# Kernel tuning notes

Hardware: AMD Instinct MI355X
Metric: run time of the kernel (lower is better)

The kernel has to match this reference:

```python
import jax, jax.numpy as jnp
import numpy as np
import math

NHEAD = 8
OUT = 64
EF = 64
IN = 256
NTYPES = 5
NH = 50000
NT = 100000
E = 800000
NEG_SLOPE = 0.2

def _uniform(key, shape, fan):
    # matches reset(): uniform(-stdv, stdv), stdv = sqrt(6/(fan_in+fan_out)) over last two dims
    stdv = math.sqrt(6.0 / (shape[-2] + shape[-1]))
    return jax.random.uniform(key, shape, jnp.float32, -stdv, stdv)

def setup_inputs() -> dict:
    key = jax.random.key(0)
    ks = jax.random.split(key, 12)
    head_feature = jax.random.normal(ks[0], (NH, IN), jnp.float32)
    tail_feature = jax.random.normal(ks[1], (NT, IN), jnp.float32)
    head_ind = jax.random.randint(ks[2], (E,), 0, NH)
    tail_ind = jax.random.randint(ks[3], (E,), 0, NT)
    tmp_edge = jax.random.randint(ks[4], (E,), 0, NTYPES)
    edge_emb = _uniform(ks[5], (NTYPES, EF), None)
    W = _uniform(ks[6], (IN, OUT * NHEAD), None)
    W_e = _uniform(ks[7], (EF, EF * NHEAD), None)
    a_l = _uniform(ks[8], (1, NHEAD, OUT), None)
    a_r = _uniform(ks[9], (1, NHEAD, OUT), None)
    a_e = _uniform(ks[10], (1, NHEAD, EF), None)
    return {"head_feature": head_feature, "tail_feature": tail_feature,
            "head_ind": head_ind, "tail_ind": tail_ind, "tmp_edge": tmp_edge,
            "edge_emb": edge_emb, "W": W, "W_e": W_e,
            "a_l": a_l, "a_r": a_r, "a_e": a_e}

def reference(head_feature, tail_feature, head_ind, tail_ind, tmp_edge,
              edge_emb, W, W_e, a_l, a_r, a_e):
    n_head_nodes = head_feature.shape[0]
    # projections (dropout is identity in eval)
    h_head = (head_feature @ W).reshape(-1, NHEAD, OUT)   # [NH, H, D]
    h_tail = (tail_feature @ W).reshape(-1, NHEAD, OUT)   # [NT, H, D]
    e = (edge_emb @ W_e).reshape(-1, NHEAD, EF)           # [T, H, EF]
    # per-edge attention logits, all heads at once: [E, H]
    h_l = jnp.sum(a_l * h_head, axis=-1)[head_ind]
    h_r = jnp.sum(a_r * h_tail, axis=-1)[tail_ind]
    h_e = jnp.sum(a_e * e, axis=-1)[tmp_edge]
    att = jax.nn.leaky_relu(h_l + h_r + h_e, NEG_SLOPE)
    # sparse (per-destination-row) softmax, vectorized over heads
    seg_max = jax.ops.segment_max(att, head_ind, num_segments=n_head_nodes)
    att = jnp.exp(att - seg_max[head_ind])
    denom = jax.ops.segment_sum(att, head_ind, num_segments=n_head_nodes)
    att = att / denom[head_ind]                           # [E, H]
    # weighted aggregation per head (small fixed loop over heads)
    outs = [jax.ops.segment_sum(att[:, n:n + 1] * h_tail[tail_ind, n, :],
                                head_ind, num_segments=n_head_nodes)
            for n in range(NHEAD)]
    out = jnp.stack(outs, axis=1).reshape(n_head_nodes, -1)  # [NH, H*D]
    return out, att
```

## Files before the change

### kernel.cpp

```cpp
#include <hip/hip_runtime.h>

#define NH 50000
#define NT 100000
#define NE 800000
#define MPAD 100096

typedef __attribute__((ext_vector_type(8))) short bf16x8;
typedef __attribute__((ext_vector_type(4))) float f32x4;

__device__ __forceinline__ unsigned short f2bf(float f){
  unsigned int u = __float_as_uint(f);
  u += 0x7FFFu + ((u >> 16) & 1u);
  return (unsigned short)(u >> 16);
}

__device__ __forceinline__ void fma8(float* acc, float w, uint4 pk){
  acc[0] += w*__uint_as_float(pk.x<<16); acc[1] += w*__uint_as_float(pk.x&0xFFFF0000u);
  acc[2] += w*__uint_as_float(pk.y<<16); acc[3] += w*__uint_as_float(pk.y&0xFFFF0000u);
  acc[4] += w*__uint_as_float(pk.z<<16); acc[5] += w*__uint_as_float(pk.z&0xFFFF0000u);
  acc[6] += w*__uint_as_float(pk.w<<16); acc[7] += w*__uint_as_float(pk.w&0xFFFF0000u);
}

__global__ void k_prep(const float* __restrict__ W, const float* __restrict__ W_e,
                       const float* __restrict__ edge_emb,
                       const float* __restrict__ a_l, const float* __restrict__ a_r,
                       const float* __restrict__ a_e,
                       unsigned short* __restrict__ wlr_t,
                       float* __restrict__ h_e){
  __shared__ float s_al[512], s_ar[512], s_ae[512], s_wef[512];
  int t = threadIdx.x;
  for (int i=t;i<512;i+=256){ s_al[i]=a_l[i]; s_ar[i]=a_r[i]; s_ae[i]=a_e[i]; }
  __syncthreads();
  { int k = t;
    for (int h=0;h<8;h++){
      float accl=0.f, accr=0.f;
      for (int d=0; d<64; d++){
        float w = W[k*512 + h*64 + d];
        accl += w*s_al[h*64+d];
        accr += w*s_ar[h*64+d];
      }
      wlr_t[h*256 + k]     = f2bf(accl);
      wlr_t[(8+h)*256 + k] = f2bf(accr);
    }
  }
  if (t<64){
    for (int h=0;h<8;h++){
      float acc=0.f;
      for (int f=0; f<64; f++) acc += W_e[t*512 + h*64 + f]*s_ae[h*64+f];
      s_wef[t*8+h]=acc;
    }
  }
  __syncthreads();
  if (t<40){
    int ty=t>>3, h=t&7;
    float acc=0.f;
    for (int k2=0;k2<64;k2++) acc += edge_emb[ty*64+k2]*s_wef[k2*8+h];
    h_e[t]=acc;
  }
}

__global__ void k_wt(const float* __restrict__ W, unsigned short* __restrict__ Wt){
  int n = blockIdx.x, k = threadIdx.x;
  Wt[n*256+k] = f2bf(W[k*512+n]);
}

__global__ __launch_bounds__(256) void k_hlr2(const float* __restrict__ head_f,
      const float* __restrict__ tail_f, const unsigned short* __restrict__ wlr_t,
      float* __restrict__ h_l, float* __restrict__ h_r){
  __shared__ unsigned short As[256*64];
  __shared__ unsigned short Bs[16*256];
  int t = threadIdx.x;
  int wave = t>>6, lane = t&63;
  int lr = lane&15, lq = lane>>4;
  long r0 = (long)blockIdx.x*256;

#pragma unroll
  for (int i=0;i<2;i++){
    int q = i*256 + t;
    int c = q>>5, un = q&31;
    float4 v = *(const float4*)(wlr_t + c*256 + un*8);
    int u = un ^ (c&7);
    *(float4*)((char*)Bs + c*512 + u*16) = v;
  }

  f32x4 acc[4];
#pragma unroll
  for (int mf=0;mf<4;mf++) acc[mf]=(f32x4){0.f,0.f,0.f,0.f};

  for (int kt=0; kt<4; kt++){
    __syncthreads();
#pragma unroll
    for (int i=0;i<16;i++){
      int q = i*256+t;
      int row = q>>4, cg = q&15;
      long gr = r0 + row;
      float4 v = make_float4(0.f,0.f,0.f,0.f);
      if (gr < NH) v = *(const float4*)(head_f + gr*256 + kt*64 + cg*4);
      else if (gr < NH+NT) v = *(const float4*)(tail_f + (gr-NH)*256 + kt*64 + cg*4);
      int u = (cg>>1) ^ (row&7);
      ushort4 sv;
      sv.x=f2bf(v.x); sv.y=f2bf(v.y); sv.z=f2bf(v.z); sv.w=f2bf(v.w);
      *(ushort4*)((char*)As + row*128 + u*16 + (cg&1)*8) = sv;
    }
    __syncthreads();
#pragma unroll
    for (int ks=0;ks<2;ks++){
      int un = kt*8 + ks*4 + lq;
      int cu = un ^ (lr&7);
      bf16x8 bfr = *(const bf16x8*)((const char*)Bs + lr*512 + cu*16);
#pragma unroll
      for (int mf=0;mf<4;mf++){
        int r = wave*64 + mf*16 + lr;
        int u = (ks*4+lq) ^ (r&7);
        bf16x8 afr = *(const bf16x8*)((const char*)As + r*128 + u*16);
        acc[mf] = __builtin_amdgcn_mfma_f32_16x16x32_bf16(afr, bfr, acc[mf], 0,0,0);
      }
    }
  }
#pragma unroll
  for (int mf=0;mf<4;mf++)
#pragma unroll
    for (int j=0;j<4;j++){
      long grow = r0 + wave*64 + mf*16 + lq*4 + j;
      float v = acc[mf][j];
      if (grow < NH){ if (lr<8) h_l[grow*8+lr] = v; }
      else if (grow < NH+NT){ if (lr>=8) h_r[(grow-NH)*8+lr-8] = v; }
    }
}

__global__ __launch_bounds__(256) void k_gemm(const float* __restrict__ Aref,
      const unsigned short* __restrict__ Wt, unsigned short* __restrict__ Cout){
  __shared__ unsigned short As[128*64];
  __shared__ unsigned short Bs[128*64];
  int t = threadIdx.x;
  int m0 = blockIdx.x*128;
  int n0 = blockIdx.y*128;
  int wave = t>>6, lane = t&63;
  int wm = (wave>>1)*64, wn = (wave&1)*64;
  int lr = lane & 15, lq = lane >> 4;

  f32x4 acc[4][4];
#pragma unroll
  for (int mf=0;mf<4;mf++)
#pragma unroll
    for (int nf=0;nf<4;nf++) acc[mf][nf] = (f32x4){0.f,0.f,0.f,0.f};

  for (int kt=0; kt<4; kt++){
#pragma unroll
    for (int i=0;i<8;i++){
      int q = i*256 + t;
      int row = q>>4;
      int cg  = q&15;
      int grow = m0 + row;
      float4 v = make_float4(0.f,0.f,0.f,0.f);
      if (grow < NT) v = *(const float4*)(Aref + (size_t)grow*256 + kt*64 + cg*4);
      int u  = (cg>>1) ^ (row&7);
      ushort4 sv;
      sv.x=f2bf(v.x); sv.y=f2bf(v.y); sv.z=f2bf(v.z); sv.w=f2bf(v.w);
      *(ushort4*)((char*)As + row*128 + u*16 + (cg&1)*8) = sv;
    }
#pragma unroll
    for (int i=0;i<4;i++){
      int q = i*256 + t;
      int row = q>>3;
      int un  = q&7;
      float4 v = *(const float4*)(Wt + (size_t)(n0+row)*256 + kt*64 + un*8);
      int u = un ^ (row&7);
      *(float4*)((char*)Bs + row*128 + u*16) = v;
    }
    __syncthreads();

    bf16x8 af[2][4], bfr[2][4];
#pragma unroll
    for (int ks=0;ks<2;ks++)
#pragma unroll
      for (int mf=0;mf<4;mf++){
        int r = wm + mf*16 + lr;
        int u = (ks*4 + lq) ^ (r&7);
        af[ks][mf] = *(const bf16x8*)((const char*)As + r*128 + u*16);
      }
#pragma unroll
    for (int ks=0;ks<2;ks++)
#pragma unroll
      for (int nf=0;nf<4;nf++){
        int c = wn + nf*16 + lr;
        int u = (ks*4 + lq) ^ (c&7);
        bfr[ks][nf] = *(const bf16x8*)((const char*)Bs + c*128 + u*16);
      }
#pragma unroll
    for (int ks=0;ks<2;ks++)
#pragma unroll
      for (int mf=0;mf<4;mf++)
#pragma unroll
        for (int nf=0;nf<4;nf++)
          acc[mf][nf] = __builtin_amdgcn_mfma_f32_16x16x32_bf16(af[ks][mf], bfr[ks][nf], acc[mf][nf], 0,0,0);
    __syncthreads();
  }
#pragma unroll
  for (int mf=0;mf<4;mf++)
#pragma unroll
    for (int nf=0;nf<4;nf++){
      int gr = m0 + wm + mf*16 + lq*4;
      int gc = n0 + wn + nf*16 + lr;
#pragma unroll
      for (int j=0;j<4;j++)
        Cout[(size_t)(gr+j)*512 + gc] = f2bf(acc[mf][nf][j]);
    }
}

__global__ void k_hist(const int* __restrict__ head_ind, int* __restrict__ cnt){
  int e = blockIdx.x*256 + threadIdx.x;
  atomicAdd(&cnt[head_ind[e]], 1);
}

__global__ void k_scan1(const int* __restrict__ cnt, int* __restrict__ bsum){
  __shared__ int s[256];
  int b=blockIdx.x, t=threadIdx.x, g=b*256+t;
  s[t] = (g<NH)? cnt[g] : 0;
  __syncthreads();
  for (int off=128; off>0; off>>=1){ if (t<off) s[t]+=s[t+off]; __syncthreads(); }
  if (t==0) bsum[b]=s[0];
}
__global__ void k_scan2(int* __restrict__ bsum, int nb){
  __shared__ int s[256];
  int t=threadIdx.x;
  int v = (t<nb)? bsum[t] : 0;
  s[t]=v; __syncthreads();
  for (int off=1; off<256; off<<=1){
    int u = (t>=off)? s[t-off] : 0; __syncthreads();
    s[t]+=u; __syncthreads();
  }
  if (t<nb) bsum[t] = s[t]-v;
}
__global__ void k_scan3(const int* __restrict__ cnt, const int* __restrict__ bsum,
                        int* __restrict__ offs, int* __restrict__ cur){
  __shared__ int s[256];
  int b=blockIdx.x, t=threadIdx.x, g=b*256+t;
  int v=(g<NH)? cnt[g] : 0;
  s[t]=v; __syncthreads();
  for (int off=1; off<256; off<<=1){
    int u=(t>=off)? s[t-off] : 0; __syncthreads();
    s[t]+=u; __syncthreads();
  }
  int excl = s[t]-v + bsum[b];
  if (g<NH){
    offs[g]=excl; cur[g]=excl;
    if (g==NH-1) offs[NH]=excl+v;
  }
}

__global__ void k_logit2(const int* __restrict__ head_ind, const int* __restrict__ tail_ind,
                         const int* __restrict__ tmp_edge,
                         const float* __restrict__ h_l, const float* __restrict__ h_r,
                         const float* __restrict__ h_e,
                         int* __restrict__ cur,
                         float* __restrict__ att, float* __restrict__ att_csr,
                         int* __restrict__ edge_of, int* __restrict__ tail_s){
  int g = blockIdx.x*256 + threadIdx.x;
  int e = g>>3, h = g&7, l = threadIdx.x&63;
  int hd = head_ind[e], tl = tail_ind[e], ty = tmp_edge[e];
  float v = h_l[hd*8+h] + h_r[tl*8+h] + h_e[ty*8+h];
  v = v > 0.f ? v : 0.2f*v;
  att[g] = v;
  int p = 0;
  if (h==0) p = atomicAdd(&cur[hd], 1);
  p = __shfl(p, l & ~7);
  att_csr[p*8+h] = v;
  if (h==0){ edge_of[p]=e; tail_s[p]=tl; }
}

__global__ __launch_bounds__(256) void k_agg3(const int* __restrict__ offs,
      const int* __restrict__ edge_of, const int* __restrict__ tail_s,
      const float* __restrict__ att_csr,
      const unsigned short* __restrict__ h_tail,
      float* __restrict__ att, float* __restrict__ out){
  int t = threadIdx.x;
  int l = t & 63;
  int i = blockIdx.x*4 + (t>>6);
  int h = l & 7, hq = l >> 3;
  int s0 = offs[i];
  int deg = offs[i+1] - s0;

  float m = -1e30f;
  for (int q = hq; q < deg; q += 8) m = fmaxf(m, att_csr[(s0+q)*8 + h]);
  m = fmaxf(m, __shfl_xor(m, 8));
  m = fmaxf(m, __shfl_xor(m, 16));
  m = fmaxf(m, __shfl_xor(m, 32));
  float sum = 0.f;
  for (int q = hq; q < deg; q += 8) sum += __expf(att_csr[(s0+q)*8 + h] - m);
  sum += __shfl_xor(sum, 8); sum += __shfl_xor(sum, 16); sum += __shfl_xor(sum, 32);
  float r = (deg > 0) ? 1.f/sum : 0.f;

  for (int q = hq; q < deg; q += 8){
    int p = s0 + q;
    float a = __expf(att_csr[p*8 + h] - m) * r;
    int e = edge_of[p];
    att[(size_t)e*8 + h] = a;
  }

  float mh = __shfl(m, hq), rh = __shfl(r, hq);
  float acc[8];
#pragma unroll
  for (int c=0;c<8;c++) acc[c]=0.f;
  int j = 0;
  for (; j+2 <= deg; j += 2){
    int p0 = s0+j, p1 = s0+j+1;
    int t0 = tail_s[p0], t1 = tail_s[p1];
    float a0 = att_csr[p0*8 + hq], a1 = att_csr[p1*8 + hq];
    uint4 r0 = *(const uint4*)(h_tail + (size_t)t0*512 + l*8);
    uint4 r1 = *(const uint4*)(h_tail + (size_t)t1*512 + l*8);
    float w0 = __expf(a0 - mh) * rh;
    float w1 = __expf(a1 - mh) * rh;
    fma8(acc, w0, r0);
    fma8(acc, w1, r1);
  }
  if (j < deg){
    int p0 = s0+j;
    int t0 = tail_s[p0];
    float a0 = att_csr[p0*8 + hq];
    uint4 r0 = *(const uint4*)(h_tail + (size_t)t0*512 + l*8);
    float w0 = __expf(a0 - mh) * rh;
    fma8(acc, w0, r0);
  }
  float* o = out + (size_t)i*512 + l*8;
  *(float4*)o     = make_float4(acc[0],acc[1],acc[2],acc[3]);
  *(float4*)(o+4) = make_float4(acc[4],acc[5],acc[6],acc[7]);
}

extern "C" void kernel_launch(void* const* d_in, const int* in_sizes, int n_in,
                              void* d_out, int out_size, void* d_ws, size_t ws_size,
                              hipStream_t stream) {
  const float* head_f   = (const float*)d_in[0];
  const float* tail_f   = (const float*)d_in[1];
  const int*   head_ind = (const int*)d_in[2];
  const int*   tail_ind = (const int*)d_in[3];
  const int*   tmp_edge = (const int*)d_in[4];
  const float* edge_emb = (const float*)d_in[5];
  const float* W        = (const float*)d_in[6];
  const float* W_e      = (const float*)d_in[7];
  const float* a_l      = (const float*)d_in[8];
  const float* a_r      = (const float*)d_in[9];
  const float* a_e      = (const float*)d_in[10];

  float* out = (float*)d_out;
  float* att = out + (size_t)NH*512;

  char* ws = (char*)d_ws;
  auto alloc = [&](size_t bytes)->char*{ char* p = ws; ws += (bytes+511)&~(size_t)511; return p; };
  unsigned short* Wt    = (unsigned short*)alloc((size_t)512*256*2);
  unsigned short* wlr_t = (unsigned short*)alloc((size_t)16*256*2);
  float* h_e            = (float*)alloc(512);
  float* h_l            = (float*)alloc((size_t)NH*8*4);
  float* h_r            = (float*)alloc((size_t)NT*8*4);
  unsigned short* h_tail= (unsigned short*)alloc((size_t)MPAD*512*2);
  int* cnt              = (int*)alloc((size_t)NH*4);
  int* offs             = (int*)alloc((size_t)(NH+1)*4);
  int* cur              = (int*)alloc((size_t)NH*4);
  int* bsum             = (int*)alloc(1024);
  int* edge_of          = (int*)alloc((size_t)NE*4);
  int* tail_s           = (int*)alloc((size_t)NE*4);
  float* att_csr        = (float*)alloc((size_t)NE*8*4);

  hipMemsetAsync(cnt, 0, (size_t)NH*4, stream);
  k_prep<<<1,256,0,stream>>>(W, W_e, edge_emb, a_l, a_r, a_e, wlr_t, h_e);
  k_wt<<<512,256,0,stream>>>(W, Wt);
  k_hlr2<<<(NH+NT+255)/256,256,0,stream>>>(head_f, tail_f, wlr_t, h_l, h_r);
  k_gemm<<<dim3(MPAD/128,4),256,0,stream>>>(tail_f, Wt, h_tail);
  k_hist<<<NE/256,256,0,stream>>>(head_ind, cnt);
  k_scan1<<<196,256,0,stream>>>(cnt, bsum);
  k_scan2<<<1,256,0,stream>>>(bsum, 196);
  k_scan3<<<196,256,0,stream>>>(cnt, bsum, offs, cur);
  k_logit2<<<NE*8/256,256,0,stream>>>(head_ind, tail_ind, tmp_edge, h_l, h_r, h_e,
                                      cur, att, att_csr, edge_of, tail_s);
  k_agg3<<<NH/4,256,0,stream>>>(offs, edge_of, tail_s, att_csr, h_tail, att, out);
}
```

Measured before the change: 465.9 us.

## Fuse tail attention logits into projection GEMM epilogue and merge att writes into aggregation

The tail-side logit h_r is now computed in the k_gemm epilogue as a dot product of the fp32 accumulators with a_r, reduced with lane shuffles. This removes the 100k tail rows from k_hlr2, so the tail features are not read a second time. The redundant att write in k_logit2 and the separate normalization pass in k_agg3 are removed; normalized weights are written with nontemporal stores inside the aggregation loop, which is unrolled to 4 edges. h_r now comes from fp32 accumulators instead of a bf16 folded weight, which slightly changes numerics. There is also a bug risk: k_gemm runs over MPAD rows and guards with gr<NT, which is fine, but one write lane per head group issues scattered stores.

```diff
diff --git a/kernel.cpp b/kernel.cpp
--- a/kernel.cpp
+++ b/kernel.cpp
@@ -64,9 +64,8 @@
   Wt[n*256+k] = f2bf(W[k*512+n]);
 }
 
-__global__ __launch_bounds__(256) void k_hlr2(const float* __restrict__ head_f,
-      const float* __restrict__ tail_f, const unsigned short* __restrict__ wlr_t,
-      float* __restrict__ h_l, float* __restrict__ h_r){
+__global__ __launch_bounds__(256) void k_hl(const float* __restrict__ head_f,
+      const unsigned short* __restrict__ wlr_t, float* __restrict__ h_l){
   __shared__ unsigned short As[256*64];
   __shared__ unsigned short Bs[16*256];
   int t = threadIdx.x;
@@ -96,7 +95,6 @@
       long gr = r0 + row;
       float4 v = make_float4(0.f,0.f,0.f,0.f);
       if (gr < NH) v = *(const float4*)(head_f + gr*256 + kt*64 + cg*4);
-      else if (gr < NH+NT) v = *(const float4*)(tail_f + (gr-NH)*256 + kt*64 + cg*4);
       int u = (cg>>1) ^ (row&7);
       ushort4 sv;
       sv.x=f2bf(v.x); sv.y=f2bf(v.y); sv.z=f2bf(v.z); sv.w=f2bf(v.w);
@@ -122,14 +120,13 @@
 #pragma unroll
     for (int j=0;j<4;j++){
       long grow = r0 + wave*64 + mf*16 + lq*4 + j;
-      float v = acc[mf][j];
-      if (grow < NH){ if (lr<8) h_l[grow*8+lr] = v; }
-      else if (grow < NH+NT){ if (lr>=8) h_r[(grow-NH)*8+lr-8] = v; }
+      if (grow < NH && lr < 8) h_l[grow*8+lr] = acc[mf][j];
     }
 }
 
 __global__ __launch_bounds__(256) void k_gemm(const float* __restrict__ Aref,
-      const unsigned short* __restrict__ Wt, unsigned short* __restrict__ Cout){
+      const unsigned short* __restrict__ Wt, const float* __restrict__ a_r_g,
+      unsigned short* __restrict__ Cout, float* __restrict__ h_r){
   __shared__ unsigned short As[128*64];
   __shared__ unsigned short Bs[128*64];
   int t = threadIdx.x;
@@ -206,6 +203,23 @@
       for (int j=0;j<4;j++)
         Cout[(size_t)(gr+j)*512 + gc] = f2bf(acc[mf][nf][j]);
     }
+  {
+    int h = (n0 + wn) >> 6;
+    float w[4];
+#pragma unroll
+    for (int nf=0;nf<4;nf++) w[nf] = a_r_g[h*64 + nf*16 + lr];
+#pragma unroll
+    for (int mf=0;mf<4;mf++)
+#pragma unroll
+      for (int j=0;j<4;j++){
+        float s = acc[mf][0][j]*w[0] + acc[mf][1][j]*w[1]
+                + acc[mf][2][j]*w[2] + acc[mf][3][j]*w[3];
+        s += __shfl_xor(s, 1); s += __shfl_xor(s, 2);
+        s += __shfl_xor(s, 4); s += __shfl_xor(s, 8);
+        int gr = m0 + wm + mf*16 + lq*4 + j;
+        if (lr == 0 && gr < NT) h_r[(size_t)gr*8 + h] = s;
+      }
+  }
 }
 
 __global__ void k_hist(const int* __restrict__ head_ind, int* __restrict__ cnt){
@@ -254,14 +268,13 @@
                          const float* __restrict__ h_l, const float* __restrict__ h_r,
                          const float* __restrict__ h_e,
                          int* __restrict__ cur,
-                         float* __restrict__ att, float* __restrict__ att_csr,
+                         float* __restrict__ att_csr,
                          int* __restrict__ edge_of, int* __restrict__ tail_s){
   int g = blockIdx.x*256 + threadIdx.x;
   int e = g>>3, h = g&7, l = threadIdx.x&63;
   int hd = head_ind[e], tl = tail_ind[e], ty = tmp_edge[e];
-  float v = h_l[hd*8+h] + h_r[tl*8+h] + h_e[ty*8+h];
+  float v = h_l[hd*8+h] + h_r[(size_t)tl*8+h] + h_e[ty*8+h];
   v = v > 0.f ? v : 0.2f*v;
-  att[g] = v;
   int p = 0;
   if (h==0) p = atomicAdd(&cur[hd], 1);
   p = __shfl(p, l & ~7);
@@ -291,40 +304,48 @@
   sum += __shfl_xor(sum, 8); sum += __shfl_xor(sum, 16); sum += __shfl_xor(sum, 32);
   float r = (deg > 0) ? 1.f/sum : 0.f;
 
-  for (int q = hq; q < deg; q += 8){
-    int p = s0 + q;
-    float a = __expf(att_csr[p*8 + h] - m) * r;
-    int e = edge_of[p];
-    att[(size_t)e*8 + h] = a;
-  }
-
   float mh = __shfl(m, hq), rh = __shfl(r, hq);
+  bool wlane = (l & 7) == 0;
   float acc[8];
 #pragma unroll
   for (int c=0;c<8;c++) acc[c]=0.f;
   int j = 0;
-  for (; j+2 <= deg; j += 2){
-    int p0 = s0+j, p1 = s0+j+1;
-    int t0 = tail_s[p0], t1 = tail_s[p1];
-    float a0 = att_csr[p0*8 + hq], a1 = att_csr[p1*8 + hq];
+  for (; j+4 <= deg; j += 4){
+    int p0=s0+j, p1=p0+1, p2=p0+2, p3=p0+3;
+    int t0=tail_s[p0], t1=tail_s[p1], t2=tail_s[p2], t3=tail_s[p3];
+    float a0=att_csr[p0*8+hq], a1=att_csr[p1*8+hq];
+    float a2=att_csr[p2*8+hq], a3=att_csr[p3*8+hq];
     uint4 r0 = *(const uint4*)(h_tail + (size_t)t0*512 + l*8);
     uint4 r1 = *(const uint4*)(h_tail + (size_t)t1*512 + l*8);
-    float w0 = __expf(a0 - mh) * rh;
-    float w1 = __expf(a1 - mh) * rh;
+    uint4 r2 = *(const uint4*)(h_tail + (size_t)t2*512 + l*8);
+    uint4 r3 = *(const uint4*)(h_tail + (size_t)t3*512 + l*8);
+    float w0=__expf(a0-mh)*rh, w1=__expf(a1-mh)*rh;
+    float w2=__expf(a2-mh)*rh, w3=__expf(a3-mh)*rh;
+    if (wlane){
+      __builtin_nontemporal_store(w0, &att[(size_t)edge_of[p0]*8 + hq]);
+      __builtin_nontemporal_store(w1, &att[(size_t)edge_of[p1]*8 + hq]);
+      __builtin_nontemporal_store(w2, &att[(size_t)edge_of[p2]*8 + hq]);
+      __builtin_nontemporal_store(w3, &att[(size_t)edge_of[p3]*8 + hq]);
+    }
     fma8(acc, w0, r0);
     fma8(acc, w1, r1);
-  }
-  if (j < deg){
+    fma8(acc, w2, r2);
+    fma8(acc, w3, r3);
+  }
+  for (; j < deg; j++){
     int p0 = s0+j;
     int t0 = tail_s[p0];
     float a0 = att_csr[p0*8 + hq];
     uint4 r0 = *(const uint4*)(h_tail + (size_t)t0*512 + l*8);
     float w0 = __expf(a0 - mh) * rh;
+    if (wlane) __builtin_nontemporal_store(w0, &att[(size_t)edge_of[p0]*8 + hq]);
     fma8(acc, w0, r0);
   }
   float* o = out + (size_t)i*512 + l*8;
-  *(float4*)o     = make_float4(acc[0],acc[1],acc[2],acc[3]);
-  *(float4*)(o+4) = make_float4(acc[4],acc[5],acc[6],acc[7]);
+  f32x4 v0 = {acc[0],acc[1],acc[2],acc[3]};
+  f32x4 v1 = {acc[4],acc[5],acc[6],acc[7]};
+  __builtin_nontemporal_store(v0, (f32x4*)o);
+  __builtin_nontemporal_store(v1, (f32x4*)(o+4));
 }
 
 extern "C" void kernel_launch(void* const* d_in, const int* in_sizes, int n_in,
@@ -364,13 +385,13 @@
   hipMemsetAsync(cnt, 0, (size_t)NH*4, stream);
   k_prep<<<1,256,0,stream>>>(W, W_e, edge_emb, a_l, a_r, a_e, wlr_t, h_e);
   k_wt<<<512,256,0,stream>>>(W, Wt);
-  k_hlr2<<<(NH+NT+255)/256,256,0,stream>>>(head_f, tail_f, wlr_t, h_l, h_r);
-  k_gemm<<<dim3(MPAD/128,4),256,0,stream>>>(tail_f, Wt, h_tail);
+  k_hl<<<(NH+255)/256,256,0,stream>>>(head_f, wlr_t, h_l);
+  k_gemm<<<dim3(MPAD/128,4),256,0,stream>>>(tail_f, Wt, a_r, h_tail, h_r);
   k_hist<<<NE/256,256,0,stream>>>(head_ind, cnt);
   k_scan1<<<196,256,0,stream>>>(cnt, bsum);
   k_scan2<<<1,256,0,stream>>>(bsum, 196);
   k_scan3<<<196,256,0,stream>>>(cnt, bsum, offs, cur);
   k_logit2<<<NE*8/256,256,0,stream>>>(head_ind, tail_ind, tmp_edge, h_l, h_r, h_e,
-                                      cur, att, att_csr, edge_of, tail_s);
+                                      cur, att_csr, edge_of, tail_s);
   k_agg3<<<NH/4,256,0,stream>>>(offs, edge_of, tail_s, att_csr, h_tail, att, out);
 }
```

New measurement: 465.6 us. About the same (-0.1%).
